# Kernel tuning notes

Hardware: AMD Instinct MI355X
Metric: run time of the kernel (lower is better)

## Reference

```python
import jax, jax.numpy as jnp
import numpy as np

_BN = 1.0 / np.sqrt(1.0 + 1e-5)  # eval-mode BatchNorm1d with default (fresh-init) stats/affine

def bn(z):
    return z * _BN

def lrelu(z, a):
    return jnp.where(z >= 0, z, a * z)

NEG = -9e15

def setup_inputs() -> dict:
    key = jax.random.key(0)
    ks = jax.random.split(key, 20)
    H = Wd = 256; B = 200; N = 2048; NHID = 128; OUT = 64; HEADS = 4
    x = jax.random.normal(ks[0], (H, Wd, B), dtype=jnp.float32)
    Q = jax.random.uniform(ks[1], (H * Wd, N), dtype=jnp.float32)
    adj = (jax.random.uniform(ks[2], (N, N)) < 0.02).astype(jnp.float32)
    adj = jnp.maximum(adj, jnp.eye(N, dtype=jnp.float32))  # self loops so no empty rows
    def u(k, shape, fan):
        s = 1.0 / np.sqrt(fan)
        return jax.random.uniform(k, shape, jnp.float32, -s, s)
    inp = dict(x=x, adj=adj, Q=Q)
    inp['g1a_W'] = u(ks[3], (B, NHID), NHID);  inp['g1a_b'] = u(ks[4], (NHID,), NHID)
    inp['g1b_W'] = u(ks[5], (NHID, B), B);     inp['g1b_b'] = u(ks[6], (B,), B)
    inp['g2a_W'] = u(ks[7], (B, NHID), NHID);  inp['g2a_b'] = u(ks[8], (NHID,), NHID)
    inp['g2b_W'] = u(ks[9], (NHID, OUT), OUT); inp['g2b_b'] = u(ks[10], (OUT,), OUT)
    inp['gat_W'] = jax.random.normal(ks[11], (HEADS, B, NHID)) * 0.1
    inp['gat_a'] = jax.random.normal(ks[12], (HEADS, 2 * NHID)) * 0.1
    inp['out_W'] = jax.random.normal(ks[13], (HEADS * NHID, OUT)) * 0.1
    inp['out_a'] = jax.random.normal(ks[14], (2 * OUT,)) * 0.1
    inp['Wf'] = u(ks[15], (2, OUT), OUT)
    inp['bf'] = u(ks[16], (2, OUT), OUT)
    inp['conv_w'] = jax.random.normal(ks[17], (3,)) * 0.5
    inp['conv_b'] = jax.random.normal(ks[18], (1,)) * 0.1
    return inp

def reference(x, adj, Q, g1a_W, g1a_b, g1b_W, g1b_b, g2a_W, g2a_b, g2b_W, g2b_b,
              gat_W, gat_a, out_W, out_a, Wf, bf, conv_w, conv_b):
    HW = x.shape[0] * x.shape[1]
    xf = x.reshape(HW, -1)                                   # [HW, C]
    normQ = Q / jnp.sum(Q, axis=0, keepdims=True)            # column-normalized assignment
    sp = normQ.T @ xf                                        # [N, C] superpixel features
    xn = bn(sp)

    # ---- Res_GCN branch ----
    def gcn_block(z, Wa, ba, Wb, bb):
        z = bn(z)
        z = lrelu(adj @ (z @ Wa) + ba, 0.01)
        z = bn(z)
        return adj @ (z @ Wb) + bb

    xg = bn(xn)
    y = lrelu(bn(gcn_block(xg, g1a_W, g1a_b, g1b_W, g1b_b)), 0.01)
    xg = xg + y
    GCN_x = lrelu(bn(gcn_block(xg, g2a_W, g2a_b, g2b_W, g2b_b)), 0.01)  # [N, OUT]

    # ---- GAT branch (fused pairwise scores: e_ij = lrelu(a1.Wh_i + a2.Wh_j)) ----
    mask = adj > 0
    nhid = gat_W.shape[2]

    def gat_head(Wk, ak):
        Wh = xn @ Wk                                         # [N, nhid]
        f1 = Wh @ ak[:nhid]                                  # [N]
        f2 = Wh @ ak[nhid:]                                  # [N]
        e = lrelu(f1[:, None] + f2[None, :], 0.2)            # [N, N]
        att = jax.nn.softmax(jnp.where(mask, e, NEG), axis=1)
        return jax.nn.elu(att @ Wh)                          # concat=True -> ELU

    heads = jax.vmap(gat_head)(gat_W, gat_a)                 # [H, N, nhid]
    hcat = jnp.moveaxis(heads, 0, 1).reshape(heads.shape[1], -1)  # [N, H*nhid]

    fo = out_W.shape[1]
    Wh = hcat @ out_W                                        # [N, OUT]
    e = lrelu((Wh @ out_a[:fo])[:, None] + (Wh @ out_a[fo:])[None, :], 0.2)
    att = jax.nn.softmax(jnp.where(mask, e, NEG), axis=1)
    GAT_x = lrelu(bn(jax.nn.elu(att @ Wh)), 0.01)            # [N, OUT]

    # ---- adaptive fusion ----
    mn = jnp.minimum(GCN_x, GAT_x)
    mx = jnp.maximum(GCN_x, GAT_x)
    avg = (GCN_x * Wf[0] + bf[0]) + (GAT_x * Wf[1] + bf[1])
    stk = jnp.stack([mn, mx, avg], axis=0)                   # [3, N, OUT]
    inp3 = stk + GAT_x + GCN_x                               # broadcast add
    y = jnp.einsum('c,cnf->nf', conv_w, inp3) + conv_b       # 1x1 conv 3->1 channels
    y = lrelu(bn(y), 0.2)                                    # AF2GNN1 leakyrelu(alpha)
    return Q @ y                                             # [HW, OUT]
```

## Files before the change

kernel.cpp:

```cpp
#include <hip/hip_runtime.h>
#include <math.h>

#define BNF 0.9999950000374997f

constexpr int N    = 2048;
constexpr int C    = 200;
constexpr int HW   = 65536;
constexpr int MAXDEG = 96;

typedef unsigned short u16;
typedef __attribute__((ext_vector_type(8))) short short8;
typedef __attribute__((ext_vector_type(4))) float f32x4;

union Frag  { short8 v; ushort4 h[2]; };
union FragA { short8 v; uint2 u2[2]; };

__device__ inline u16 f2bf(float x) {
    unsigned int u = __float_as_uint(x);
    unsigned int r = (u + 0x7fffu + ((u >> 16) & 1u)) >> 16;
    return (u16)r;
}

__device__ __forceinline__ void gload16(const void* g, void* l) {
    __builtin_amdgcn_global_load_lds(
        (const __attribute__((address_space(1))) unsigned int*)g,
        (__attribute__((address_space(3))) unsigned int*)l, 16, 0, 0);
}

__global__ __launch_bounds__(256) void k_convX(const float* __restrict__ xf,
                                               u16* __restrict__ xfT,
                                               const float* __restrict__ adj,
                                               int* __restrict__ deg,
                                               int* __restrict__ idxs) {
    const int t = threadIdx.x;
    if (blockIdx.x >= 512) {
        int w = t >> 6, lane = t & 63;
        int n = (blockIdx.x - 512) * 4 + w;
        const float* row = adj + (size_t)n * N;
        int base = 0;
        for (int c = 0; c < N; c += 64) {
            float v = row[c + lane];
            bool p = v > 0.f;
            unsigned long long m = __ballot(p);
            int pos = __popcll(m & ((1ull << lane) - 1ull));
            if (p && (base + pos) < MAXDEG)
                idxs[(size_t)n * MAXDEG + base + pos] = c + lane;
            base += __popcll(m);
        }
        if (lane == 0) deg[n] = base < MAXDEG ? base : MAXDEG;
        return;
    }
    __shared__ __align__(16) u16 T2[200][140];
    const int i0 = blockIdx.x * 128;
    for (int p = 0; p < 25; ++p) {
        int idx = p * 256 + t;
        int il = idx / 50, cq = idx % 50;
        float4 v = *(const float4*)&xf[(size_t)(i0 + il) * 200 + cq * 4];
        T2[cq * 4 + 0][il] = f2bf(v.x);
        T2[cq * 4 + 1][il] = f2bf(v.y);
        T2[cq * 4 + 2][il] = f2bf(v.z);
        T2[cq * 4 + 3][il] = f2bf(v.w);
    }
    __syncthreads();
    for (int p = 0; p < 13; ++p) {
        int c = p * 16 + (t >> 4);
        if (c < 200) {
            int io = (t & 15) * 8;
            u16* dst = &xfT[(size_t)c * 65536 + i0 + io];
            *(ushort4*)&dst[0] = *(const ushort4*)&T2[c][io];
            *(ushort4*)&dst[4] = *(const ushort4*)&T2[c][io + 4];
        }
    }
    ushort4 z4 = {0, 0, 0, 0};
    for (int idx = t; idx < 8 * 16; idx += 256) {
        int r = 200 + (idx >> 4), io = (idx & 15) * 8;
        u16* dst = &xfT[(size_t)r * 65536 + i0 + io];
        *(ushort4*)&dst[0] = z4;
        *(ushort4*)&dst[4] = z4;
    }
}

__global__ __launch_bounds__(256, 3) void k_bigS(const float* __restrict__ Q,
                                                 const u16* __restrict__ xfT,
                                                 u16* __restrict__ Qbf,
                                                 float* __restrict__ S_part,
                                                 float* __restrict__ csPart) {
    __shared__ __align__(16) u16 Bt[2][208 * 32];
    __shared__ __align__(16) u16 At[64 * 34];
    const int bid = blockIdx.x;
    const int xcd = bid & 7, jb = bid >> 3;
    const int nt_b = jb & 31;
    const int ks_b = ((jb >> 5) << 3) + xcd;
    const int n0 = nt_b * 64;
    const size_t i0 = (size_t)ks_b * 2048;
    const int t = threadIdx.x, w = t >> 6, l = t & 63;
    const int ct0 = (w == 0) ? 0 : (4 + (w - 1) * 3);
    const int nct = (w == 0) ? 4 : 3;
    const int lrowB = l >> 2;
    const int scolB = (((l & 3) ^ ((l >> 3) & 3)) << 3);
    const int nq = t & 15;
    const int kp = t >> 4;

    f32x4 acc[4][4];
#pragma unroll
    for (int a = 0; a < 4; ++a)
#pragma unroll
        for (int b = 0; b < 4; ++b) acc[a][b] = (f32x4){0.f, 0.f, 0.f, 0.f};
    float csum[4] = {0.f, 0.f, 0.f, 0.f};

    float4 aq0, ar0, aq1, ar1;

#define ISSUE_B(PAR, STEP)                                                      \
    {                                                                           \
        const size_t kc = i0 + (size_t)(STEP) * 32 + scolB;                     \
        for (int s = w; s < 13; s += 4)                                         \
            gload16(&xfT[(size_t)(s * 16 + lrowB) * 65536 + kc],                \
                    &Bt[PAR][s * 512]);                                         \
    }

#define LOAD_A(AQ, AR, STEP)                                                    \
    {                                                                           \
        const float* qp = &Q[(i0 + (size_t)(STEP) * 32 + kp * 2) * 2048         \
                             + n0 + nq * 4];                                    \
        AQ = *(const float4*)qp;                                                \
        AR = *(const float4*)(qp + 2048);                                       \
    }

#define WRITE_A(AQ, AR, STEP)                                                   \
    {                                                                           \
        const float* ca = (const float*)&AQ;                                    \
        const float* cb = (const float*)&AR;                                    \
        ushort4 s0, s1;                                                         \
        u16* q0 = (u16*)&s0; u16* q1 = (u16*)&s1;                               \
        _Pragma("unroll")                                                       \
        for (int jj = 0; jj < 4; ++jj) {                                        \
            const int n_ = nq * 4 + jj;                                         \
            ushort2 p2;                                                         \
            p2.x = f2bf(ca[jj]); p2.y = f2bf(cb[jj]);                           \
            *(ushort2*)&At[n_ * 34 + ((n_ & 1) << 1) + kp * 2] = p2;            \
            csum[jj] += ca[jj] + cb[jj];                                        \
            q0[jj] = p2.x; q1[jj] = p2.y;                                       \
        }                                                                       \
        const size_t r0 = i0 + (size_t)(STEP) * 32 + kp * 2;                    \
        *(ushort4*)&Qbf[r0 * 2048 + n0 + nq * 4] = s0;                          \
        *(ushort4*)&Qbf[(r0 + 1) * 2048 + n0 + nq * 4] = s1;                    \
    }

#define MFMA_PHASE(PAR)                                                         \
    {                                                                           \
        const u16* Bb = Bt[PAR];                                                \
        const int g = l >> 4;                                                   \
        FragA af[4];                                                            \
        _Pragma("unroll")                                                       \
        for (int nt = 0; nt < 4; ++nt) {                                        \
            const int r = nt * 16 + (l & 15);                                   \
            const int ab = r * 34 + ((r & 1) << 1) + g * 8;                     \
            af[nt].u2[0] = *(const uint2*)&At[ab];                              \
            af[nt].u2[1] = *(const uint2*)&At[ab + 4];                          \
        }                                                                       \
        _Pragma("unroll")                                                       \
        for (int c = 0; c < 4; ++c) {                                           \
            if (c < nct) {                                                      \
                const int rb = (ct0 + c) * 16 + (l & 15);                       \
                Frag bf;                                                        \
                bf.v = *(const short8*)&Bb[rb * 32 + ((g ^ ((rb >> 1) & 3)) << 3)]; \
                _Pragma("unroll")                                               \
                for (int nt = 0; nt < 4; ++nt)                                  \
                    acc[nt][c] = __builtin_amdgcn_mfma_f32_16x16x32_bf16(       \
                        af[nt].v, bf.v, acc[nt][c], 0, 0, 0);                   \
            }                                                                   \
        }                                                                       \
    }

#define STEPBODY(STEP, PAR, NPAR, CQ, CR, COND)                                 \
    {                                                                           \
        if (COND) ISSUE_B(NPAR, (STEP) + 1);                                    \
        WRITE_A(CQ, CR, STEP);                                                  \
        {                                                                       \
            const int nst = ((STEP) + 2 > 63) ? 63 : (STEP) + 2;                \
            LOAD_A(CQ, CR, nst);                                                \
        }                                                                       \
        asm volatile("s_waitcnt lgkmcnt(0)" ::: "memory");                      \
        __builtin_amdgcn_s_barrier();                                           \
        if (COND) {                                                             \
            if (w == 0) asm volatile("s_waitcnt vmcnt(12)" ::: "memory");       \
            else        asm volatile("s_waitcnt vmcnt(11)" ::: "memory");       \
        } else {                                                                \
            asm volatile("s_waitcnt vmcnt(0)" ::: "memory");                    \
        }                                                                       \
        MFMA_PHASE(PAR);                                                        \
        __builtin_amdgcn_s_barrier();                                           \
    }

    ISSUE_B(0, 0);
    LOAD_A(aq0, ar0, 0);
    LOAD_A(aq1, ar1, 1);

    for (int s2 = 0; s2 < 32; ++s2) {
        STEPBODY(s2 * 2,     0, 1, aq0, ar0, true);
        STEPBODY(s2 * 2 + 1, 1, 0, aq1, ar1, (s2 < 31));
    }
#undef STEPBODY
#undef MFMA_PHASE
#undef WRITE_A
#undef LOAD_A
#undef ISSUE_B

    __syncthreads();
    float* csF = (float*)At;
#pragma unroll
    for (int jj = 0; jj < 4; ++jj)
        csF[kp * 64 + nq * 4 + jj] = csum[jj];
    __syncthreads();
    if (t < 64) {
        float s = 0.f;
#pragma unroll
        for (int g2 = 0; g2 < 16; ++g2) s += csF[g2 * 64 + t];
        csPart[(size_t)ks_b * 2048 + n0 + t] = s;
    }
    float* Sp = S_part + (size_t)ks_b * 409600;
#pragma unroll
    for (int nt = 0; nt < 4; ++nt)
#pragma unroll
        for (int c = 0; c < 4; ++c) {
            if (c < nct) {
                const int cc = (ct0 + c) * 16 + (l & 15);
                if (cc < 200) {
                    const int nbase = n0 + nt * 16 + ((l >> 4) << 2);
#pragma unroll
                    for (int r = 0; r < 4; ++r)
                        Sp[(size_t)(nbase + r) * 200 + cc] = acc[nt][c][r];
                }
            }
        }
}

__global__ void k_redS(const float* __restrict__ S_part, const float* __restrict__ csPart,
                       float* __restrict__ xn, float* __restrict__ xg) {
    int i = blockIdx.x * 256 + threadIdx.x;
    if (i >= N * C) return;
    int n = i / C;
    float s = 0.f, csn = 0.f;
#pragma unroll 8
    for (int p = 0; p < 32; ++p) s += S_part[(size_t)p * 409600 + i];
#pragma unroll 8
    for (int p = 0; p < 32; ++p) csn += csPart[(size_t)p * 2048 + n];
    float v = BNF * s / csn;
    xn[i] = v;
    xg[i] = BNF * v;
}

__global__ __launch_bounds__(256) void k_mm(const float* __restrict__ A,
                                            const float* __restrict__ W,
                                            float* __restrict__ Cc,
                                            int K, int Wout, int ostride,
                                            int zc_off, int zw_str, float scale) {
    __shared__ float ldsA[32][33];
    __shared__ float ldsW[32][64];
    const int rt = blockIdx.x * 32;
    const int ct = blockIdx.y * 64;
    const int z  = blockIdx.z;
    const float* Wp = W + (size_t)z * zw_str;
    const int coff = z * zc_off;
    const int t = threadIdx.x;
    const int lane = t & 63, wg = t >> 6;
    float acc[8];
#pragma unroll
    for (int r = 0; r < 8; ++r) acc[r] = 0.f;

    for (int k0 = 0; k0 < K; k0 += 32) {
        for (int idx = t; idx < 32 * 32; idx += 256) {
            int r = idx >> 5, kk = idx & 31;
            int k = k0 + kk;
            ldsA[r][kk] = (k < K) ? A[(size_t)(rt + r) * K + k] : 0.f;
        }
        for (int idx = t; idx < 32 * 64; idx += 256) {
            int kk = idx >> 6, c = idx & 63;
            int k = k0 + kk, cg = ct + c;
            ldsW[kk][c] = (k < K && cg < Wout) ? Wp[(size_t)k * Wout + cg] : 0.f;
        }
        __syncthreads();
#pragma unroll 8
        for (int kk = 0; kk < 32; ++kk) {
            float wv = ldsW[kk][lane];
#pragma unroll
            for (int r = 0; r < 8; ++r) acc[r] += ldsA[wg * 8 + r][kk] * wv;
        }
        __syncthreads();
    }
    int cg = ct + lane;
    if (cg < Wout) {
#pragma unroll
        for (int r = 0; r < 8; ++r)
            Cc[(size_t)(rt + wg * 8 + r) * ostride + coff + cg] = scale * acc[r];
    }
}

__global__ void k_spmm(const float* __restrict__ h, const int* __restrict__ deg,
                       const int* __restrict__ idxs, const float* __restrict__ bias,
                       const float* __restrict__ res, float* __restrict__ out,
                       int W, float s, int act) {
    int n = blockIdx.x;
    int d = deg[n];
    const int* row = idxs + (size_t)n * MAXDEG;
    int k0 = threadIdx.x;
    int k1 = threadIdx.x + 128;
    float a0 = 0.f, a1 = 0.f;
    for (int j = 0; j < d; ++j) {
        const float* hr = h + (size_t)row[j] * W;
        a0 += hr[k0];
        if (k1 < W) a1 += hr[k1];
    }
    {
        float v = s * (a0 + bias[k0]);
        if (act) v = v >= 0.f ? v : 0.01f * v;
        if (res) v += res[(size_t)n * W + k0];
        out[(size_t)n * W + k0] = v;
    }
    if (k1 < W) {
        float v = s * (a1 + bias[k1]);
        if (act) v = v >= 0.f ? v : 0.01f * v;
        if (res) v += res[(size_t)n * W + k1];
        out[(size_t)n * W + k1] = v;
    }
}

__global__ __launch_bounds__(256) void k_wh5(const float* __restrict__ xn,
                                             const float* __restrict__ gatW,
                                             const float* __restrict__ gata,
                                             const float* __restrict__ g1aW,
                                             float* __restrict__ WhB,
                                             float* __restrict__ f1,
                                             float* __restrict__ f2,
                                             float* __restrict__ hbuf) {
    __shared__ float ldsA[32][33];
    __shared__ float ldsW[32][128];
    __shared__ float ldsWh[32][129];
    const int rt = blockIdx.x * 32;
    const int z  = blockIdx.y;
    const bool gat = z < 4;
    const float* Wp = gat ? gatW + (size_t)z * 25600 : g1aW;
    const int t = threadIdx.x;
    const int col = t & 127, rg = t >> 7;
    float acc[16];
#pragma unroll
    for (int r = 0; r < 16; ++r) acc[r] = 0.f;

    for (int k0 = 0; k0 < 200; k0 += 32) {
        for (int idx = t; idx < 32 * 32; idx += 256) {
            int r = idx >> 5, kk = idx & 31;
            int k = k0 + kk;
            ldsA[r][kk] = (k < 200) ? xn[(size_t)(rt + r) * 200 + k] : 0.f;
        }
        for (int idx = t; idx < 32 * 128; idx += 256) {
            int kk = idx >> 7, c = idx & 127;
            int k = k0 + kk;
            ldsW[kk][c] = (k < 200) ? Wp[(size_t)k * 128 + c] : 0.f;
        }
        __syncthreads();
#pragma unroll 8
        for (int kk = 0; kk < 32; ++kk) {
            float wv = ldsW[kk][col];
#pragma unroll
            for (int r = 0; r < 16; ++r) acc[r] += ldsA[rg * 16 + r][kk] * wv;
        }
        __syncthreads();
    }
    if (gat) {
#pragma unroll
        for (int r = 0; r < 16; ++r) {
            ldsWh[rg * 16 + r][col] = acc[r];
            WhB[(size_t)(rt + rg * 16 + r) * 512 + z * 128 + col] = acc[r];
        }
        __syncthreads();
        int row = t >> 3, p = t & 7;
        const float* a = gata + z * 256;
        float s1 = 0.f, s2 = 0.f;
#pragma unroll
        for (int j = 0; j < 16; ++j) {
            int c = p * 16 + j;
            float v = ldsWh[row][c];
            s1 += v * a[c]; s2 += v * a[128 + c];
        }
        s1 += __shfl_xor(s1, 1); s1 += __shfl_xor(s1, 2); s1 += __shfl_xor(s1, 4);
        s2 += __shfl_xor(s2, 1); s2 += __shfl_xor(s2, 2); s2 += __shfl_xor(s2, 4);
        if (p == 0) { f1[z * N + rt + row] = s1; f2[z * N + rt + row] = s2; }
    } else {
        const float sc = BNF * BNF;
#pragma unroll
        for (int r = 0; r < 16; ++r)
            hbuf[(size_t)(rt + rg * 16 + r) * 128 + col] = sc * acc[r];
    }
}

__global__ void k_s1ah(const float* __restrict__ hbuf, const int* __restrict__ deg,
                       const int* __restrict__ idxs, const float* __restrict__ g1ab,
                       float* __restrict__ zbuf, const float* __restrict__ WhB,
                       const float* __restrict__ f1, const float* __restrict__ f2,
                       float* __restrict__ hcat) {
    __shared__ float eW[256];
    const int vb = blockIdx.x;
    const int t = threadIdx.x;
    if (vb < 1024) {
        const int n = vb * 2 + (t >> 7), k = t & 127;
        const int d = deg[n];
        const int* row = idxs + (size_t)n * MAXDEG;
        float a = 0.f;
        for (int j = 0; j < d; ++j) a += hbuf[(size_t)row[j] * 128 + k];
        float v = a + g1ab[k];
        v = v >= 0.f ? v : 0.01f * v;
        zbuf[(size_t)n * 128 + k] = v;
    } else {
        const int va = vb - 1024;
        const int half = t >> 7, k = t & 127;
        const int u = va * 2 + half;
        const int h = u >> 11, n = u & 2047;
        const int d = deg[n];
        const int* row = idxs + (size_t)n * MAXDEG;
        const float f1v = f1[h * N + n];
        const float* f2h = f2 + h * N;
        float* e = eW + half * 128;
        if (k < d) {
            float ev = f1v + f2h[row[k]];
            e[k] = ev >= 0.f ? ev : 0.2f * ev;
        }
        __syncthreads();
        float mx = -1e30f;
        for (int j = 0; j < d; ++j) mx = fmaxf(mx, e[j]);
        __syncthreads();
        if (k < d) e[k] = __expf(e[k] - mx);
        __syncthreads();
        float ssum = 0.f, acc = 0.f;
        for (int j = 0; j < d; ++j) ssum += e[j];
        for (int j = 0; j < d; ++j)
            acc += e[j] * WhB[(size_t)row[j] * 512 + h * 128 + k];
        float v = acc / ssum;
        v = v > 0.f ? v : __expf(v) - 1.f;
        hcat[(size_t)n * 512 + h * 128 + k] = v;
    }
}

__global__ __launch_bounds__(256) void k_g1bO(const float* __restrict__ zbuf,
                                              const float* __restrict__ g1bW,
                                              float* __restrict__ hbuf,
                                              const float* __restrict__ hcat,
                                              const float* __restrict__ outW,
                                              const float* __restrict__ outa,
                                              float* __restrict__ WhO,
                                              float* __restrict__ f1o,
                                              float* __restrict__ f2o) {
    __shared__ float ldsA[32][33];
    __shared__ float ldsW[32][65];
    const int vb = blockIdx.x;
    const int t = threadIdx.x;
    const int lane = t & 63, wg = t >> 6;
    float acc[8];
#pragma unroll
    for (int r = 0; r < 8; ++r) acc[r] = 0.f;

    if (vb < 256) {
        const int rt = (vb & 63) * 32, ct = (vb >> 6) * 64;
        for (int k0 = 0; k0 < 128; k0 += 32) {
            for (int idx = t; idx < 1024; idx += 256) {
                int r = idx >> 5, kk = idx & 31;
                ldsA[r][kk] = zbuf[(size_t)(rt + r) * 128 + k0 + kk];
            }
            for (int idx = t; idx < 2048; idx += 256) {
                int kk = idx >> 6, c = idx & 63;
                int cg = ct + c;
                ldsW[kk][c] = (cg < 200) ? g1bW[(size_t)(k0 + kk) * 200 + cg] : 0.f;
            }
            __syncthreads();
#pragma unroll 8
            for (int kk = 0; kk < 32; ++kk) {
                float wv = ldsW[kk][lane];
#pragma unroll
                for (int r = 0; r < 8; ++r) acc[r] += ldsA[wg * 8 + r][kk] * wv;
            }
            __syncthreads();
        }
        int cg = ct + lane;
        if (cg < 200) {
#pragma unroll
            for (int r = 0; r < 8; ++r)
                hbuf[(size_t)(rt + wg * 8 + r) * 200 + cg] = BNF * acc[r];
        }
    } else {
        const int rt = (vb - 256) * 32;
        for (int k0 = 0; k0 < 512; k0 += 32) {
            for (int idx = t; idx < 1024; idx += 256) {
                int r = idx >> 5, kk = idx & 31;
                ldsA[r][kk] = hcat[(size_t)(rt + r) * 512 + k0 + kk];
            }
            for (int idx = t; idx < 2048; idx += 256) {
                int kk = idx >> 6, c = idx & 63;
                ldsW[kk][c] = outW[(size_t)(k0 + kk) * 64 + c];
            }
            __syncthreads();
#pragma unroll 8
            for (int kk = 0; kk < 32; ++kk) {
                float wv = ldsW[kk][lane];
#pragma unroll
                for (int r = 0; r < 8; ++r) acc[r] += ldsA[wg * 8 + r][kk] * wv;
            }
            __syncthreads();
        }
#pragma unroll
        for (int r = 0; r < 8; ++r)
            WhO[(size_t)(rt + wg * 8 + r) * 64 + lane] = acc[r];
#pragma unroll
        for (int r = 0; r < 8; ++r) {
            float v1 = acc[r] * outa[lane];
            float v2 = acc[r] * outa[64 + lane];
#pragma unroll
            for (int off = 32; off; off >>= 1) {
                v1 += __shfl_down(v1, off);
                v2 += __shfl_down(v2, off);
            }
            if (lane == 0) { f1o[rt + wg * 8 + r] = v1; f2o[rt + wg * 8 + r] = v2; }
        }
    }
}

__global__ void k_att_out(const float* __restrict__ WhO, const float* __restrict__ f1o,
                          const float* __restrict__ f2o, const int* __restrict__ deg,
                          const int* __restrict__ idxs, const float* __restrict__ GCNx,
                          const float* __restrict__ Wf, const float* __restrict__ bfp,
                          const float* __restrict__ cw, const float* __restrict__ cb,
                          u16* __restrict__ yT) {
    __shared__ float eW[MAXDEG];
    int n = blockIdx.x;
    int k = threadIdx.x;
    int d = deg[n];
    const int* row = idxs + (size_t)n * MAXDEG;
    float f1v = f1o[n];
    for (int j = k; j < d; j += 64) {
        float e = f1v + f2o[row[j]];
        eW[j] = e >= 0.f ? e : 0.2f * e;
    }
    __syncthreads();
    float mx = -1e30f;
    for (int j = 0; j < d; ++j) mx = fmaxf(mx, eW[j]);
    __syncthreads();
    for (int j = k; j < d; j += 64) eW[j] = __expf(eW[j] - mx);
    __syncthreads();
    float ssum = 0.f, acc = 0.f;
    for (int j = 0; j < d; ++j) ssum += eW[j];
    for (int j = 0; j < d; ++j)
        acc += eW[j] * WhO[(size_t)row[j] * 64 + k];
    float v = acc / ssum;
    v = v > 0.f ? v : __expf(v) - 1.f;
    v *= BNF;
    float gat = v >= 0.f ? v : 0.01f * v;
    float g = GCNx[(size_t)n * 64 + k];
    float mn = fminf(g, gat), mxv = fmaxf(g, gat);
    float avg = g * Wf[k] + bfp[k] + gat * Wf[64 + k] + bfp[64 + k];
    float base = g + gat;
    float yv = cw[0] * (mn + base) + cw[1] * (mxv + base) + cw[2] * (avg + base) + cb[0];
    yv *= BNF;
    yv = yv >= 0.f ? yv : 0.2f * yv;
    yT[k * 2048 + n] = f2bf(yv);
}

__global__ __launch_bounds__(256, 2) void k_final(const u16* __restrict__ Qbf,
                                                  const u16* __restrict__ yT,
                                                  float* __restrict__ out) {
    __shared__ __align__(16) u16 Aq[3][128 * 64];
    __shared__ __align__(16) u16 By[3][64 * 64];
    const int i0 = blockIdx.x * 128;
    const int t = threadIdx.x, w = t >> 6, l = t & 63;
    const int lrow = l >> 3;
    const int scol = (((l & 7) ^ ((l >> 3) & 7)) << 3);
    f32x4 acc[2][4];
#pragma unroll
    for (int a = 0; a < 2; ++a)
#pragma unroll
        for (int b = 0; b < 4; ++b) acc[a][b] = (f32x4){0.f, 0.f, 0.f, 0.f};

#define STAGE_F(buf, step)                                                          \
    {                                                                               \
        const size_t kc = (size_t)(step) * 64 + scol;                               \
        for (int s = w; s < 16; s += 4)                                             \
            gload16(&Qbf[(size_t)(i0 + s * 8 + lrow) * 2048 + kc],                  \
                    &Aq[buf][s * 512]);                                             \
        for (int s = w; s < 8; s += 4)                                              \
            gload16(&yT[(size_t)(s * 8 + lrow) * 2048 + kc],                        \
                    &By[buf][s * 512]);                                             \
    }

    STAGE_F(0, 0);
    STAGE_F(1, 1);
    for (int step = 0; step < 32; ++step) {
        const int cur = step % 3;
        if (step + 2 < 32) STAGE_F((step + 2) % 3, step + 2);
        if (step + 2 < 32)      asm volatile("s_waitcnt vmcnt(12)" ::: "memory");
        else if (step + 1 < 32) asm volatile("s_waitcnt vmcnt(6)"  ::: "memory");
        else                    asm volatile("s_waitcnt vmcnt(0)"  ::: "memory");
        __builtin_amdgcn_s_barrier();

        const u16* Ab = Aq[cur];
        const u16* Bb = By[cur];
#pragma unroll
        for (int sub = 0; sub < 2; ++sub) {
            const int c8 = sub * 4 + (l >> 4);
            Frag a[2];
#pragma unroll
            for (int it = 0; it < 2; ++it) {
                const int r = w * 32 + it * 16 + (l & 15);
                a[it].v = *(const short8*)&Ab[r * 64 + ((c8 ^ (r & 7)) << 3)];
            }
#pragma unroll
            for (int ft = 0; ft < 4; ++ft) {
                const int rb = ft * 16 + (l & 15);
                Frag b;
                b.v = *(const short8*)&Bb[rb * 64 + ((c8 ^ (rb & 7)) << 3)];
#pragma unroll
                for (int it = 0; it < 2; ++it)
                    acc[it][ft] = __builtin_amdgcn_mfma_f32_16x16x32_bf16(
                        a[it].v, b.v, acc[it][ft], 0, 0, 0);
            }
        }
        asm volatile("s_waitcnt lgkmcnt(0)" ::: "memory");
        __builtin_amdgcn_s_barrier();
    }
#undef STAGE_F
#pragma unroll
    for (int it = 0; it < 2; ++it)
#pragma unroll
        for (int ft = 0; ft < 4; ++ft) {
            const int i = i0 + w * 32 + it * 16 + ((l >> 4) << 2);
            const int f = ft * 16 + (l & 15);
#pragma unroll
            for (int r = 0; r < 4; ++r)
                out[(size_t)(i + r) * 64 + f] = acc[it][ft][r];
        }
}

extern "C" void kernel_launch(void* const* d_in, const int* in_sizes, int n_in,
                              void* d_out, int out_size, void* d_ws, size_t ws_size,
                              hipStream_t stream) {
    const float* x     = (const float*)d_in[0];
    const float* adj   = (const float*)d_in[1];
    const float* Q     = (const float*)d_in[2];
    const float* g1aW  = (const float*)d_in[3];
    const float* g1ab  = (const float*)d_in[4];
    const float* g1bW  = (const float*)d_in[5];
    const float* g1bb  = (const float*)d_in[6];
    const float* g2aW  = (const float*)d_in[7];
    const float* g2ab  = (const float*)d_in[8];
    const float* g2bW  = (const float*)d_in[9];
    const float* g2bb  = (const float*)d_in[10];
    const float* gatW  = (const float*)d_in[11];
    const float* gata  = (const float*)d_in[12];
    const float* outW  = (const float*)d_in[13];
    const float* outa  = (const float*)d_in[14];
    const float* Wf    = (const float*)d_in[15];
    const float* bfp   = (const float*)d_in[16];
    const float* convw = (const float*)d_in[17];
    const float* convb = (const float*)d_in[18];

    float* ws   = (float*)d_ws;
    float* xn   = ws + 411648;
    float* xg   = ws + 821248;
    float* xg2  = ws + 1230848;
    float* hbuf = ws + 1640448;
    float* zbuf = ws + 2050048;
    float* WhO  = ws + 2312192;
    float* GCNx = ws + 2443264;
    float* f1   = ws + 2836480;
    float* f2   = ws + 2844672;
    float* f1o  = ws + 2852864;
    float* f2o  = ws + 2854912;
    int*   deg  = (int*)(ws + 2856960);
    int*   idxs = (int*)(ws + 2859008);
    u16*   yT   = (u16*)(ws + 1640448);
    float* csPart = ws + 3600000;
    float* S_part = ws + 4200000;
    u16*   Qbf    = (u16*)(ws + 71308864);
    u16*   xfT    = (u16*)(ws + 138417728);

    float* out  = (float*)d_out;
    float* WhB  = out;
    float* hcat = out + 1048576;

    k_convX<<<1024, 256, 0, stream>>>(x, xfT, adj, deg, idxs);
    k_bigS<<<1024, 256, 0, stream>>>(Q, xfT, Qbf, S_part, csPart);
    k_redS<<<1600, 256, 0, stream>>>(S_part, csPart, xn, xg);

    k_wh5<<<dim3(64, 5), 256, 0, stream>>>(xn, gatW, gata, g1aW, WhB, f1, f2, hbuf);

    k_s1ah<<<5120, 256, 0, stream>>>(hbuf, deg, idxs, g1ab, zbuf, WhB, f1, f2, hcat);
    k_g1bO<<<320, 256, 0, stream>>>(zbuf, g1bW, hbuf, hcat, outW, outa, WhO, f1o, f2o);

    k_spmm<<<N, 128, 0, stream>>>(hbuf, deg, idxs, g1bb, xg, xg2, 200, BNF, 1);
    k_mm<<<dim3(64, 2, 1), 256, 0, stream>>>(xg2, g2aW, hbuf, 200, 128, 128, 0, 0, BNF);
    k_spmm<<<N, 128, 0, stream>>>(hbuf, deg, idxs, g2ab, nullptr, zbuf, 128, 1.f, 1);
    k_mm<<<dim3(64, 1, 1), 256, 0, stream>>>(zbuf, g2bW, hbuf, 128, 64, 64, 0, 0, BNF);
    k_spmm<<<N, 64, 0, stream>>>(hbuf, deg, idxs, g2bb, nullptr, GCNx, 64, BNF, 1);

    k_att_out<<<N, 64, 0, stream>>>(WhO, f1o, f2o, deg, idxs, GCNx,
                                    Wf, bfp, convw, convb, yT);

    k_final<<<512, 256, 0, stream>>>(Qbf, yT, out);
}
```

Before: 683.4 us.

## Fuse GCN spmm+matmul stages and rebalance MFMA work across waves in bigS

The big superpixel GEMM kernel now gives each of the four waves exactly 13 MFMA tiles, instead of one wave doing 16 and the others 12, which removes the imbalance at every step. In the tail, the separate sparse-aggregation and dense-matmul kernels of the second GCN block are fused pairwise into k_s2g2a and k_s3g2b. The last aggregation is folded into the attention-output kernel, which also packs four nodes per block. This cuts launches and intermediate round trips (xg, xg2, GCNx), but the fused kernels launch only 128 blocks, so they risk low occupancy.

Result: slower. 919.1 us (+34.5%).

```diff
diff --git a/kernel.cpp b/kernel.cpp
--- a/kernel.cpp
+++ b/kernel.cpp
@@ -94,18 +94,15 @@
     const int n0 = nt_b * 64;
     const size_t i0 = (size_t)ks_b * 2048;
     const int t = threadIdx.x, w = t >> 6, l = t & 63;
-    const int ct0 = (w == 0) ? 0 : (4 + (w - 1) * 3);
-    const int nct = (w == 0) ? 4 : 3;
+    const int ctlo = (w * 13) >> 2;
     const int lrowB = l >> 2;
     const int scolB = (((l & 3) ^ ((l >> 3) & 3)) << 3);
     const int nq = t & 15;
     const int kp = t >> 4;
 
-    f32x4 acc[4][4];
-#pragma unroll
-    for (int a = 0; a < 4; ++a)
-#pragma unroll
-        for (int b = 0; b < 4; ++b) acc[a][b] = (f32x4){0.f, 0.f, 0.f, 0.f};
+    f32x4 acc[13];
+#pragma unroll
+    for (int a = 0; a < 13; ++a) acc[a] = (f32x4){0.f, 0.f, 0.f, 0.f};
     float csum[4] = {0.f, 0.f, 0.f, 0.f};
 
     float4 aq0, ar0, aq1, ar1;
@@ -146,6 +143,16 @@
         *(ushort4*)&Qbf[(r0 + 1) * 2048 + n0 + nq * 4] = s1;                    \
     }
 
+#define MFMA13(W)                                                               \
+    {                                                                           \
+        _Pragma("unroll")                                                       \
+        for (int p = 0; p < 13; ++p) {                                          \
+            const int q = (W) + p;                                              \
+            acc[p] = __builtin_amdgcn_mfma_f32_16x16x32_bf16(                   \
+                af[q & 3].v, bf[q >> 2].v, acc[p], 0, 0, 0);                    \
+        }                                                                       \
+    }
+
 #define MFMA_PHASE(PAR)                                                         \
     {                                                                           \
         const u16* Bb = Bt[PAR];                                                \
@@ -158,17 +165,17 @@
             af[nt].u2[0] = *(const uint2*)&At[ab];                              \
             af[nt].u2[1] = *(const uint2*)&At[ab + 4];                          \
         }                                                                       \
+        Frag bf[4];                                                             \
         _Pragma("unroll")                                                       \
-        for (int c = 0; c < 4; ++c) {                                           \
-            if (c < nct) {                                                      \
-                const int rb = (ct0 + c) * 16 + (l & 15);                       \
-                Frag bf;                                                        \
-                bf.v = *(const short8*)&Bb[rb * 32 + ((g ^ ((rb >> 1) & 3)) << 3)]; \
-                _Pragma("unroll")                                               \
-                for (int nt = 0; nt < 4; ++nt)                                  \
-                    acc[nt][c] = __builtin_amdgcn_mfma_f32_16x16x32_bf16(       \
-                        af[nt].v, bf.v, acc[nt][c], 0, 0, 0);                   \
-            }                                                                   \
+        for (int j = 0; j < 4; ++j) {                                           \
+            const int rb = (ctlo + j) * 16 + (l & 15);                          \
+            bf[j].v = *(const short8*)&Bb[rb * 32 + ((g ^ ((rb >> 1) & 3)) << 3)]; \
+        }                                                                       \
+        switch (w) {                                                            \
+            case 0: MFMA13(0); break;                                           \
+            case 1: MFMA13(1); break;                                           \
+            case 2: MFMA13(2); break;                                           \
+            default: MFMA13(3); break;                                          \
         }                                                                       \
     }
 
@@ -202,6 +209,7 @@
     }
 #undef STEPBODY
 #undef MFMA_PHASE
+#undef MFMA13
 #undef WRITE_A
 #undef LOAD_A
 #undef ISSUE_B
@@ -220,23 +228,20 @@
     }
     float* Sp = S_part + (size_t)ks_b * 409600;
 #pragma unroll
-    for (int nt = 0; nt < 4; ++nt)
-#pragma unroll
-        for (int c = 0; c < 4; ++c) {
-            if (c < nct) {
-                const int cc = (ct0 + c) * 16 + (l & 15);
-                if (cc < 200) {
-                    const int nbase = n0 + nt * 16 + ((l >> 4) << 2);
-#pragma unroll
-                    for (int r = 0; r < 4; ++r)
-                        Sp[(size_t)(nbase + r) * 200 + cc] = acc[nt][c][r];
-                }
-            }
-        }
+    for (int p = 0; p < 13; ++p) {
+        const int q = w + p;
+        const int cc = (ctlo + (q >> 2)) * 16 + (l & 15);
+        if (cc < 200) {
+            const int nbase = n0 + (q & 3) * 16 + ((l >> 4) << 2);
+#pragma unroll
+            for (int r = 0; r < 4; ++r)
+                Sp[(size_t)(nbase + r) * 200 + cc] = acc[p][r];
+        }
+    }
 }
 
 __global__ void k_redS(const float* __restrict__ S_part, const float* __restrict__ csPart,
-                       float* __restrict__ xn, float* __restrict__ xg) {
+                       float* __restrict__ xn) {
     int i = blockIdx.x * 256 + threadIdx.x;
     if (i >= N * C) return;
     int n = i / C;
@@ -245,84 +250,7 @@
     for (int p = 0; p < 32; ++p) s += S_part[(size_t)p * 409600 + i];
 #pragma unroll 8
     for (int p = 0; p < 32; ++p) csn += csPart[(size_t)p * 2048 + n];
-    float v = BNF * s / csn;
-    xn[i] = v;
-    xg[i] = BNF * v;
-}
-
-__global__ __launch_bounds__(256) void k_mm(const float* __restrict__ A,
-                                            const float* __restrict__ W,
-                                            float* __restrict__ Cc,
-                                            int K, int Wout, int ostride,
-                                            int zc_off, int zw_str, float scale) {
-    __shared__ float ldsA[32][33];
-    __shared__ float ldsW[32][64];
-    const int rt = blockIdx.x * 32;
-    const int ct = blockIdx.y * 64;
-    const int z  = blockIdx.z;
-    const float* Wp = W + (size_t)z * zw_str;
-    const int coff = z * zc_off;
-    const int t = threadIdx.x;
-    const int lane = t & 63, wg = t >> 6;
-    float acc[8];
-#pragma unroll
-    for (int r = 0; r < 8; ++r) acc[r] = 0.f;
-
-    for (int k0 = 0; k0 < K; k0 += 32) {
-        for (int idx = t; idx < 32 * 32; idx += 256) {
-            int r = idx >> 5, kk = idx & 31;
-            int k = k0 + kk;
-            ldsA[r][kk] = (k < K) ? A[(size_t)(rt + r) * K + k] : 0.f;
-        }
-        for (int idx = t; idx < 32 * 64; idx += 256) {
-            int kk = idx >> 6, c = idx & 63;
-            int k = k0 + kk, cg = ct + c;
-            ldsW[kk][c] = (k < K && cg < Wout) ? Wp[(size_t)k * Wout + cg] : 0.f;
-        }
-        __syncthreads();
-#pragma unroll 8
-        for (int kk = 0; kk < 32; ++kk) {
-            float wv = ldsW[kk][lane];
-#pragma unroll
-            for (int r = 0; r < 8; ++r) acc[r] += ldsA[wg * 8 + r][kk] * wv;
-        }
-        __syncthreads();
-    }
-    int cg = ct + lane;
-    if (cg < Wout) {
-#pragma unroll
-        for (int r = 0; r < 8; ++r)
-            Cc[(size_t)(rt + wg * 8 + r) * ostride + coff + cg] = scale * acc[r];
-    }
-}
-
-__global__ void k_spmm(const float* __restrict__ h, const int* __restrict__ deg,
-                       const int* __restrict__ idxs, const float* __restrict__ bias,
-                       const float* __restrict__ res, float* __restrict__ out,
-                       int W, float s, int act) {
-    int n = blockIdx.x;
-    int d = deg[n];
-    const int* row = idxs + (size_t)n * MAXDEG;
-    int k0 = threadIdx.x;
-    int k1 = threadIdx.x + 128;
-    float a0 = 0.f, a1 = 0.f;
-    for (int j = 0; j < d; ++j) {
-        const float* hr = h + (size_t)row[j] * W;
-        a0 += hr[k0];
-        if (k1 < W) a1 += hr[k1];
-    }
-    {
-        float v = s * (a0 + bias[k0]);
-        if (act) v = v >= 0.f ? v : 0.01f * v;
-        if (res) v += res[(size_t)n * W + k0];
-        out[(size_t)n * W + k0] = v;
-    }
-    if (k1 < W) {
-        float v = s * (a1 + bias[k1]);
-        if (act) v = v >= 0.f ? v : 0.01f * v;
-        if (res) v += res[(size_t)n * W + k1];
-        out[(size_t)n * W + k1] = v;
-    }
+    xn[i] = BNF * s / csn;
 }
 
 __global__ __launch_bounds__(256) void k_wh5(const float* __restrict__ xn,
@@ -522,37 +450,161 @@
     }
 }
 
-__global__ void k_att_out(const float* __restrict__ WhO, const float* __restrict__ f1o,
-                          const float* __restrict__ f2o, const int* __restrict__ deg,
-                          const int* __restrict__ idxs, const float* __restrict__ GCNx,
-                          const float* __restrict__ Wf, const float* __restrict__ bfp,
-                          const float* __restrict__ cw, const float* __restrict__ cb,
-                          u16* __restrict__ yT) {
-    __shared__ float eW[MAXDEG];
-    int n = blockIdx.x;
-    int k = threadIdx.x;
-    int d = deg[n];
+__global__ __launch_bounds__(256) void k_s2g2a(const float* __restrict__ hbuf,
+                                               const int* __restrict__ deg,
+                                               const int* __restrict__ idxs,
+                                               const float* __restrict__ g1bb,
+                                               const float* __restrict__ xn,
+                                               const float* __restrict__ g2aW,
+                                               float* __restrict__ outp) {
+    __shared__ float X[16][204];
+    __shared__ float ldsW[32][128];
+    const int rt = blockIdx.x * 16;
+    const int t = threadIdx.x;
+    {
+        const int row = t >> 4, tc = t & 15;
+        const int n = rt + row;
+        const int d = deg[n];
+        const int* rp = idxs + (size_t)n * MAXDEG;
+        float a[13];
+#pragma unroll
+        for (int c = 0; c < 13; ++c) a[c] = 0.f;
+        for (int j = 0; j < d; ++j) {
+            const float* hr = hbuf + (size_t)rp[j] * 200;
+#pragma unroll
+            for (int c = 0; c < 13; ++c) {
+                int col = tc + 16 * c;
+                if (col < 200) a[c] += hr[col];
+            }
+        }
+#pragma unroll
+        for (int c = 0; c < 13; ++c) {
+            int col = tc + 16 * c;
+            if (col < 200) {
+                float v = BNF * (a[c] + g1bb[col]);
+                v = v >= 0.f ? v : 0.01f * v;
+                v += BNF * xn[(size_t)n * 200 + col];
+                X[row][col] = v;
+            }
+        }
+    }
+    __syncthreads();
+    const int col = t & 127, rg = t >> 7;
+    float acc[8];
+#pragma unroll
+    for (int r = 0; r < 8; ++r) acc[r] = 0.f;
+    for (int k0 = 0; k0 < 200; k0 += 32) {
+        for (int idx = t; idx < 4096; idx += 256) {
+            int kk = idx >> 7, c = idx & 127;
+            int k = k0 + kk;
+            ldsW[kk][c] = (k < 200) ? g2aW[(size_t)k * 128 + c] : 0.f;
+        }
+        __syncthreads();
+#pragma unroll 8
+        for (int kk = 0; kk < 32; ++kk) {
+            if (k0 + kk < 200) {
+                float wv = ldsW[kk][col];
+#pragma unroll
+                for (int r = 0; r < 8; ++r) acc[r] += X[rg * 8 + r][k0 + kk] * wv;
+            }
+        }
+        __syncthreads();
+    }
+#pragma unroll
+    for (int r = 0; r < 8; ++r)
+        outp[(size_t)(rt + rg * 8 + r) * 128 + col] = BNF * acc[r];
+}
+
+__global__ __launch_bounds__(256) void k_s3g2b(const float* __restrict__ inp,
+                                               const int* __restrict__ deg,
+                                               const int* __restrict__ idxs,
+                                               const float* __restrict__ g2ab,
+                                               const float* __restrict__ g2bW,
+                                               float* __restrict__ outp) {
+    __shared__ float Z[16][132];
+    __shared__ float ldsW[32][65];
+    const int rt = blockIdx.x * 16;
+    const int t = threadIdx.x;
+    {
+        const int row = t >> 4, tc = t & 15;
+        const int n = rt + row;
+        const int d = deg[n];
+        const int* rp = idxs + (size_t)n * MAXDEG;
+        float a[8];
+#pragma unroll
+        for (int c = 0; c < 8; ++c) a[c] = 0.f;
+        for (int j = 0; j < d; ++j) {
+            const float* hr = inp + (size_t)rp[j] * 128;
+#pragma unroll
+            for (int c = 0; c < 8; ++c) a[c] += hr[tc + 16 * c];
+        }
+#pragma unroll
+        for (int c = 0; c < 8; ++c) {
+            int col = tc + 16 * c;
+            float v = a[c] + g2ab[col];
+            Z[row][col] = v >= 0.f ? v : 0.01f * v;
+        }
+    }
+    __syncthreads();
+    const int lane = t & 63, wg = t >> 6;
+    float acc[4];
+#pragma unroll
+    for (int r = 0; r < 4; ++r) acc[r] = 0.f;
+    for (int k0 = 0; k0 < 128; k0 += 32) {
+        for (int idx = t; idx < 2048; idx += 256) {
+            int kk = idx >> 6, c = idx & 63;
+            ldsW[kk][c] = g2bW[(size_t)(k0 + kk) * 64 + c];
+        }
+        __syncthreads();
+#pragma unroll 8
+        for (int kk = 0; kk < 32; ++kk) {
+            float wv = ldsW[kk][lane];
+#pragma unroll
+            for (int r = 0; r < 4; ++r) acc[r] += Z[wg * 4 + r][k0 + kk] * wv;
+        }
+        __syncthreads();
+    }
+#pragma unroll
+    for (int r = 0; r < 4; ++r)
+        outp[(size_t)(rt + wg * 4 + r) * 64 + lane] = BNF * acc[r];
+}
+
+__global__ void k_s4ao(const float* __restrict__ h64, const int* __restrict__ deg,
+                       const int* __restrict__ idxs, const float* __restrict__ g2bb,
+                       const float* __restrict__ WhO, const float* __restrict__ f1o,
+                       const float* __restrict__ f2o,
+                       const float* __restrict__ Wf, const float* __restrict__ bfp,
+                       const float* __restrict__ cw, const float* __restrict__ cb,
+                       u16* __restrict__ yT) {
+    __shared__ float eW[4][MAXDEG];
+    const int sub = threadIdx.x >> 6, k = threadIdx.x & 63;
+    const int n = blockIdx.x * 4 + sub;
+    const int d = deg[n];
     const int* row = idxs + (size_t)n * MAXDEG;
-    float f1v = f1o[n];
+    float a = 0.f;
+    for (int j = 0; j < d; ++j) a += h64[(size_t)row[j] * 64 + k];
+    float g = a + g2bb[k];
+    g = g >= 0.f ? g : 0.01f * g;
+    g *= BNF;
+    const float f1v = f1o[n];
+    float* e = eW[sub];
     for (int j = k; j < d; j += 64) {
-        float e = f1v + f2o[row[j]];
-        eW[j] = e >= 0.f ? e : 0.2f * e;
+        float ev = f1v + f2o[row[j]];
+        e[j] = ev >= 0.f ? ev : 0.2f * ev;
     }
     __syncthreads();
     float mx = -1e30f;
-    for (int j = 0; j < d; ++j) mx = fmaxf(mx, eW[j]);
+    for (int j = 0; j < d; ++j) mx = fmaxf(mx, e[j]);
     __syncthreads();
-    for (int j = k; j < d; j += 64) eW[j] = __expf(eW[j] - mx);
+    for (int j = k; j < d; j += 64) e[j] = __expf(e[j] - mx);
     __syncthreads();
     float ssum = 0.f, acc = 0.f;
-    for (int j = 0; j < d; ++j) ssum += eW[j];
-    for (int j = 0; j < d; ++j)
-        acc += eW[j] * WhO[(size_t)row[j] * 64 + k];
+    for (int j = 0; j < d; ++j) ssum += e[j];
+    for (int j = 0; j < d; ++j) acc += e[j] * WhO[(size_t)row[j] * 64 + k];
     float v = acc / ssum;
     v = v > 0.f ? v : __expf(v) - 1.f;
     v *= BNF;
     float gat = v >= 0.f ? v : 0.01f * v;
-    float g = GCNx[(size_t)n * 64 + k];
     float mn = fminf(g, gat), mxv = fmaxf(g, gat);
     float avg = g * Wf[k] + bfp[k] + gat * Wf[64 + k] + bfp[64 + k];
     float base = g + gat;
@@ -661,19 +713,16 @@
 
     float* ws   = (float*)d_ws;
     float* xn   = ws + 411648;
-    float* xg   = ws + 821248;
-    float* xg2  = ws + 1230848;
     float* hbuf = ws + 1640448;
     float* zbuf = ws + 2050048;
     float* WhO  = ws + 2312192;
-    float* GCNx = ws + 2443264;
     float* f1   = ws + 2836480;
     float* f2   = ws + 2844672;
     float* f1o  = ws + 2852864;
     float* f2o  = ws + 2854912;
     int*   deg  = (int*)(ws + 2856960);
     int*   idxs = (int*)(ws + 2859008);
-    u16*   yT   = (u16*)(ws + 1640448);
+    u16*   yT   = (u16*)(ws + 3300000);
     float* csPart = ws + 3600000;
     float* S_part = ws + 4200000;
     u16*   Qbf    = (u16*)(ws + 71308864);
@@ -685,20 +734,14 @@
 
     k_convX<<<1024, 256, 0, stream>>>(x, xfT, adj, deg, idxs);
     k_bigS<<<1024, 256, 0, stream>>>(Q, xfT, Qbf, S_part, csPart);
-    k_redS<<<1600, 256, 0, stream>>>(S_part, csPart, xn, xg);
+    k_redS<<<1600, 256, 0, stream>>>(S_part, csPart, xn);
 
     k_wh5<<<dim3(64, 5), 256, 0, stream>>>(xn, gatW, gata, g1aW, WhB, f1, f2, hbuf);
-
     k_s1ah<<<5120, 256, 0, stream>>>(hbuf, deg, idxs, g1ab, zbuf, WhB, f1, f2, hcat);
     k_g1bO<<<320, 256, 0, stream>>>(zbuf, g1bW, hbuf, hcat, outW, outa, WhO, f1o, f2o);
-
-    k_spmm<<<N, 128, 0, stream>>>(hbuf, deg, idxs, g1bb, xg, xg2, 200, BNF, 1);
-    k_mm<<<dim3(64, 2, 1), 256, 0, stream>>>(xg2, g2aW, hbuf, 200, 128, 128, 0, 0, BNF);
-    k_spmm<<<N, 128, 0, stream>>>(hbuf, deg, idxs, g2ab, nullptr, zbuf, 128, 1.f, 1);
-    k_mm<<<dim3(64, 1, 1), 256, 0, stream>>>(zbuf, g2bW, hbuf, 128, 64, 64, 0, 0, BNF);
-    k_spmm<<<N, 64, 0, stream>>>(hbuf, deg, idxs, g2bb, nullptr, GCNx, 64, BNF, 1);
-
-    k_att_out<<<N, 64, 0, stream>>>(WhO, f1o, f2o, deg, idxs, GCNx,
+    k_s2g2a<<<128, 256, 0, stream>>>(hbuf, deg, idxs, g1bb, xn, g2aW, zbuf);
+    k_s3g2b<<<128, 256, 0, stream>>>(zbuf, deg, idxs, g2ab, g2bW, hbuf);
+    k_s4ao<<<512, 256, 0, stream>>>(hbuf, deg, idxs, g2bb, WhO, f1o, f2o,
                                     Wf, bfp, convw, convb, yT);
 
     k_final<<<512, 256, 0, stream>>>(Qbf, yT, out);
```
